# Kernel optimization log

Hardware: AMD Instinct MI355X
Metric: run time of the kernel (lower is better)

## Reference

```python
import jax, jax.numpy as jnp
import numpy as np

B, CIN, H, W = 128, 64, 32, 32
COUT, K, STRIDE, PAD = 64, 3, 1, 1
HO = (H + 2 * PAD - K) // STRIDE + 1
WO = (W + 2 * PAD - K) // STRIDE + 1


def setup_inputs() -> dict:
    key = jax.random.key(0)
    k1, k2 = jax.random.split(key)
    x = jax.random.normal(k1, (B, CIN, H, W), dtype=jnp.float32)
    # weight scaled like torch init: randn / sqrt(k*k*Cin) (orthogonal_ in torch just
    # re-orthogonalizes; scale here matches the fan-in normalization)
    weight = jax.random.normal(k2, (HO, WO, COUT, CIN, K, K), dtype=jnp.float32) / np.sqrt(K * K * CIN)
    bias = jnp.full((COUT, HO, WO), 0.5, dtype=jnp.float32)
    return {"x": x, "weight": weight, "bias": bias}


def reference(x, weight, bias):
    # pad spatial dims
    xp = jnp.pad(x, ((0, 0), (0, 0), (PAD, PAD), (PAD, PAD)))
    # gather row windows: [B, C, Ho, K, Wp]
    ri = (jnp.arange(HO) * STRIDE)[:, None] + jnp.arange(K)[None, :]  # [Ho, K]
    ci = (jnp.arange(WO) * STRIDE)[:, None] + jnp.arange(K)[None, :]  # [Wo, K]
    rows = xp[:, :, ri, :]           # [B, C, Ho, K, Wp]
    patches = rows[:, :, :, :, ci]   # [B, C, Ho, K, Wo, K]
    # per-location matmul: b c h p w q , h w d c p q -> b d h w
    out = jnp.einsum('bchpwq,hwdcpq->bdhw', patches, weight)
    return out + bias[None]
```

## Files before the change

kernel.cpp:

```cpp
#include <hip/hip_runtime.h>
#include <hip/hip_bf16.h>

#define KT 576

typedef __attribute__((ext_vector_type(8))) short  short8;
typedef __attribute__((ext_vector_type(4))) float  f32x4;

#define VMCNT(n) asm volatile("s_waitcnt vmcnt(" #n ")" ::: "memory")
#define SB() __builtin_amdgcn_sched_barrier(0)

__device__ __forceinline__ unsigned short f2bf(float f) {
  union { float f; unsigned int u; } v; v.f = f;
  return (unsigned short)((v.u + 0x7FFFu + ((v.u >> 16) & 1u)) >> 16);
}

__global__ __launch_bounds__(256) void xC2_kernel(const float* __restrict__ x,
                                                  unsigned short* __restrict__ xC2) {
  const int hp = blockIdx.x, bb = blockIdx.y, t = threadIdx.x;
  __shared__ unsigned short tile[32 * 1024];
  const bool interior = (hp >= 1 && hp <= 32);
  if (interior) {
#pragma unroll 4
    for (int i = 0; i < 32; ++i) {
      const int row = i * 32 + (t >> 3);
      const int bl = row >> 6, c = row & 63;
      const int k = t & 7;
      const float4 v = *(const float4*)(x + ((size_t)(bb * 16 + bl) * 64 + c) * 1024 +
                                        (hp - 1) * 32 + k * 4);
      const int base = (k * 4) * 1024 + (c >> 3) * 128 + bl * 8 + (c & 7);
      tile[base]        = f2bf(v.x);
      tile[base + 1024] = f2bf(v.y);
      tile[base + 2048] = f2bf(v.z);
      tile[base + 3072] = f2bf(v.w);
    }
  }
  __syncthreads();
  unsigned short* dst = xC2 + (size_t)hp * 278528 + (size_t)bb * 1024;
  const uint4 z = make_uint4(0u, 0u, 0u, 0u);
  for (int idx = t; idx < 34 * 128; idx += 256) {
    const int wp = idx >> 7, s = idx & 127;
    uint4 v = z;
    if (interior && wp >= 1 && wp <= 32) v = *(const uint4*)&tile[(wp - 1) * 1024 + s * 8];
    *(uint4*)(dst + (size_t)wp * 8192 + s * 8) = v;
  }
}

__global__ __launch_bounds__(256, 1) void lc_main(const float* __restrict__ Wt,
                                                  const float* __restrict__ bias,
                                                  const unsigned short* __restrict__ xC2,
                                                  float* __restrict__ out) {
  __shared__ unsigned short Wl[2][32 * KT];
  __shared__ float blds[128];

  const int bid = (int)blockIdx.x;
  const int swz = (bid & 7) * 64 + (bid >> 3);
  const int h = swz >> 4, rem = swz & 15, wq = rem >> 1, half = rem & 1;
  const int t = threadIdx.x, lane = t & 63, wv = t >> 6;
  const int l15 = lane & 15, lg = lane >> 4;

  if (t < 128)
    blds[t] = bias[(half * 32 + (t & 31)) * 1024 + h * 32 + wq * 4 + (t >> 5)];

  const unsigned short* xA = xC2 + (size_t)wv * 2048 + lg * 128 + l15 * 8;
  const int x7 = l15 & 7;
  const int wrow0 = l15 * KT;
  const int wrow1 = (16 + l15) * KT;

  f32x4 acc[4][2][2];
#pragma unroll
  for (int j = 0; j < 4; ++j)
#pragma unroll
    for (int bt = 0; bt < 2; ++bt)
#pragma unroll
      for (int dt = 0; dt < 2; ++dt) acc[j][bt][dt] = (f32x4){0.f, 0.f, 0.f, 0.f};

  short8 As0[3][3], As1[3][3];
  float4 wreg[18];

#define ISSUE_W(jj)                                                           \
  {                                                                           \
    const float* ws = Wt + (size_t)(h * 32 + wq * 4 + (jj)) * (64 * KT) +     \
                      (size_t)half * (32 * KT);                               \
    _Pragma("unroll")                                                         \
    for (int i = 0; i < 18; ++i) {                                            \
      const float4* p = (const float4*)ws + (i * 256 + t);                    \
      asm volatile("global_load_dwordx4 %0, %1, off" : "=v"(wreg[i]) : "v"(p)); \
    }                                                                         \
  }

#define ISSUE_A(K)                                                            \
  {                                                                           \
    _Pragma("unroll")                                                         \
    for (int s = 0; s < 3; ++s) {                                             \
      const int step = ((K) % 6) * 3 + s;                                     \
      const int pq = step >> 1, p = pq / 3, q = pq - p * 3;                   \
      const size_t off = (size_t)(h + p) * 278528 +                           \
                         (size_t)(wq * 4 + (K) / 6 + q) * 8192 + (step & 1) * 512; \
      const short8* p0 = (const short8*)(xA + off);                           \
      const short8* p1 = (const short8*)(xA + off + 1024);                    \
      asm volatile("global_load_dwordx4 %0, %1, off" : "=v"(As0[(K) % 3][s]) : "v"(p0)); \
      asm volatile("global_load_dwordx4 %0, %1, off" : "=v"(As1[(K) % 3][s]) : "v"(p1)); \
    }                                                                         \
  }

#define SCATTER(buf)                                                          \
  {                                                                           \
    _Pragma("unroll")                                                         \
    for (int i = 0; i < 18; ++i) {                                            \
      const int f = (i * 256 + t) * 4;                                        \
      const int d = (((unsigned)(f >> 6)) * 7282u) >> 16;                     \
      int kn = f - d * 576;                                                   \
      int c = ((unsigned)kn * 7282u) >> 16;                                   \
      int r = kn - c * 9;                                                     \
      const float vv[4] = {wreg[i].x, wreg[i].y, wreg[i].z, wreg[i].w};       \
      _Pragma("unroll")                                                       \
      for (int jx = 0; jx < 4; ++jx) {                                        \
        const int kp = r * 64 + c;                                            \
        const int slot = (kp >> 3) ^ (d & 7);                                 \
        Wl[buf][d * KT + slot * 8 + (kp & 7)] = f2bf(vv[jx]);                 \
        if (++r == 9) { r = 0; ++c; }                                         \
      }                                                                       \
    }                                                                         \
  }

#define STEP(jj, gg, NN)                                                      \
  {                                                                           \
    VMCNT(NN);                                                                \
    SB();                                                                     \
    _Pragma("unroll")                                                         \
    for (int s = 0; s < 3; ++s) {                                             \
      const int sb = ((gg) * 3 + s) * 4 + lg;                                 \
      const short8 b0 = *(const short8*)&Wl[(jj) & 1][wrow0 + ((sb ^ x7) << 3)]; \
      const short8 b1 = *(const short8*)&Wl[(jj) & 1][wrow1 + ((sb ^ x7) << 3)]; \
      acc[(jj)][0][0] = __builtin_amdgcn_mfma_f32_16x16x32_bf16(As0[((jj) * 6 + (gg)) % 3][s], b0, acc[(jj)][0][0], 0, 0, 0); \
      acc[(jj)][1][0] = __builtin_amdgcn_mfma_f32_16x16x32_bf16(As1[((jj) * 6 + (gg)) % 3][s], b0, acc[(jj)][1][0], 0, 0, 0); \
      acc[(jj)][0][1] = __builtin_amdgcn_mfma_f32_16x16x32_bf16(As0[((jj) * 6 + (gg)) % 3][s], b1, acc[(jj)][0][1], 0, 0, 0); \
      acc[(jj)][1][1] = __builtin_amdgcn_mfma_f32_16x16x32_bf16(As1[((jj) * 6 + (gg)) % 3][s], b1, acc[(jj)][1][1], 0, 0, 0); \
    }                                                                         \
  }

  ISSUE_W(0);
  ISSUE_A(0); ISSUE_A(1); ISSUE_A(2);
  VMCNT(18);
  SB();
  SCATTER(0);
  __syncthreads();

  ISSUE_W(1);
  STEP(0, 0, 30); ISSUE_A(3);
  STEP(0, 1, 30); ISSUE_A(4);
  STEP(0, 2, 30); ISSUE_A(5);
  STEP(0, 3, 12); ISSUE_A(6);
  STEP(0, 4, 12); ISSUE_A(7);
  STEP(0, 5, 12); ISSUE_A(8);
  SCATTER(1);
  __syncthreads();

  ISSUE_W(2);
  STEP(1, 0, 30); ISSUE_A(9);
  STEP(1, 1, 30); ISSUE_A(10);
  STEP(1, 2, 30); ISSUE_A(11);
  STEP(1, 3, 12); ISSUE_A(12);
  STEP(1, 4, 12); ISSUE_A(13);
  STEP(1, 5, 12); ISSUE_A(14);
  SCATTER(0);
  __syncthreads();

  ISSUE_W(3);
  STEP(2, 0, 30); ISSUE_A(15);
  STEP(2, 1, 30); ISSUE_A(16);
  STEP(2, 2, 30); ISSUE_A(17);
  STEP(2, 3, 12); ISSUE_A(18);
  STEP(2, 4, 12); ISSUE_A(19);
  STEP(2, 5, 12); ISSUE_A(20);
  SCATTER(1);
  __syncthreads();

  STEP(3, 0, 12); ISSUE_A(21);
  STEP(3, 1, 12); ISSUE_A(22);
  STEP(3, 2, 12); ISSUE_A(23);
  STEP(3, 3, 12);
  STEP(3, 4, 6);
  STEP(3, 5, 0);

#pragma unroll
  for (int dt = 0; dt < 2; ++dt) {
    const int dd = dt * 16 + l15;
    const int dg = half * 32 + dd;
    const float bv0 = blds[dd], bv1 = blds[32 + dd], bv2 = blds[64 + dd], bv3 = blds[96 + dd];
#pragma unroll
    for (int bt = 0; bt < 2; ++bt) {
#pragma unroll
      for (int i = 0; i < 4; ++i) {
        const int b = wv * 32 + bt * 16 + lg * 4 + i;
        float4 v;
        v.x = acc[0][bt][dt][i] + bv0;
        v.y = acc[1][bt][dt][i] + bv1;
        v.z = acc[2][bt][dt][i] + bv2;
        v.w = acc[3][bt][dt][i] + bv3;
        *(float4*)(out + (size_t)b * 65536 + (size_t)dg * 1024 + h * 32 + wq * 4) = v;
      }
    }
  }
}

extern "C" void kernel_launch(void* const* d_in, const int* in_sizes, int n_in,
                              void* d_out, int out_size, void* d_ws, size_t ws_size,
                              hipStream_t stream) {
  const float* x    = (const float*)d_in[0];
  const float* wt   = (const float*)d_in[1];
  const float* bias = (const float*)d_in[2];
  float* out        = (float*)d_out;
  unsigned short* xC2 = (unsigned short*)d_ws;

  xC2_kernel<<<dim3(34, 8), 256, 0, stream>>>(x, xC2);
  lc_main<<<512, 256, 0, stream>>>(wt, bias, xC2, out);
}
```

Baseline: 68.54 us.

## Split output channels into quarters per block to double grid and occupancy

Each block now covers 16 output channels instead of 32, so the grid doubles to 1024 blocks with half the LDS, half the weight registers, and launch bounds allowing two blocks per CU. The weight slice per block halves, and the wait counts are adjusted for the smaller weight issue. The cost is that the activation (A) fragments are now loaded twice as often across blocks, since each block reloads the same x tiles for fewer output channels.

```diff
diff --git a/kernel.cpp b/kernel.cpp
--- a/kernel.cpp
+++ b/kernel.cpp
@@ -45,44 +45,41 @@
   }
 }
 
-__global__ __launch_bounds__(256, 1) void lc_main(const float* __restrict__ Wt,
+__global__ __launch_bounds__(256, 2) void lc_main(const float* __restrict__ Wt,
                                                   const float* __restrict__ bias,
                                                   const unsigned short* __restrict__ xC2,
                                                   float* __restrict__ out) {
-  __shared__ unsigned short Wl[2][32 * KT];
-  __shared__ float blds[128];
+  __shared__ unsigned short Wl[2][16 * KT];
+  __shared__ float blds[64];
 
   const int bid = (int)blockIdx.x;
-  const int swz = (bid & 7) * 64 + (bid >> 3);
-  const int h = swz >> 4, rem = swz & 15, wq = rem >> 1, half = rem & 1;
+  const int swz = (bid & 7) * 128 + (bid >> 3);
+  const int quad = swz & 3, wq = (swz >> 2) & 7, h = swz >> 5;
   const int t = threadIdx.x, lane = t & 63, wv = t >> 6;
   const int l15 = lane & 15, lg = lane >> 4;
 
-  if (t < 128)
-    blds[t] = bias[(half * 32 + (t & 31)) * 1024 + h * 32 + wq * 4 + (t >> 5)];
+  if (t < 64)
+    blds[t] = bias[(quad * 16 + (t & 15)) * 1024 + h * 32 + wq * 4 + (t >> 4)];
 
   const unsigned short* xA = xC2 + (size_t)wv * 2048 + lg * 128 + l15 * 8;
   const int x7 = l15 & 7;
-  const int wrow0 = l15 * KT;
-  const int wrow1 = (16 + l15) * KT;
-
-  f32x4 acc[4][2][2];
+  const int wrow = l15 * KT;
+
+  f32x4 acc[4][2];
 #pragma unroll
   for (int j = 0; j < 4; ++j)
 #pragma unroll
-    for (int bt = 0; bt < 2; ++bt)
-#pragma unroll
-      for (int dt = 0; dt < 2; ++dt) acc[j][bt][dt] = (f32x4){0.f, 0.f, 0.f, 0.f};
+    for (int bt = 0; bt < 2; ++bt) acc[j][bt] = (f32x4){0.f, 0.f, 0.f, 0.f};
 
   short8 As0[3][3], As1[3][3];
-  float4 wreg[18];
+  float4 wreg[9];
 
 #define ISSUE_W(jj)                                                           \
   {                                                                           \
-    const float* ws = Wt + (size_t)(h * 32 + wq * 4 + (jj)) * (64 * KT) +     \
-                      (size_t)half * (32 * KT);                               \
-    _Pragma("unroll")                                                         \
-    for (int i = 0; i < 18; ++i) {                                            \
+    const float* ws = Wt + ((size_t)(h * 32 + wq * 4 + (jj)) * 64 +           \
+                            quad * 16) * KT;                                  \
+    _Pragma("unroll")                                                         \
+    for (int i = 0; i < 9; ++i) {                                             \
       const float4* p = (const float4*)ws + (i * 256 + t);                    \
       asm volatile("global_load_dwordx4 %0, %1, off" : "=v"(wreg[i]) : "v"(p)); \
     }                                                                         \
@@ -106,7 +103,7 @@
 #define SCATTER(buf)                                                          \
   {                                                                           \
     _Pragma("unroll")                                                         \
-    for (int i = 0; i < 18; ++i) {                                            \
+    for (int i = 0; i < 9; ++i) {                                             \
       const int f = (i * 256 + t) * 4;                                        \
       const int d = (((unsigned)(f >> 6)) * 7282u) >> 16;                     \
       int kn = f - d * 576;                                                   \
@@ -130,12 +127,9 @@
     _Pragma("unroll")                                                         \
     for (int s = 0; s < 3; ++s) {                                             \
       const int sb = ((gg) * 3 + s) * 4 + lg;                                 \
-      const short8 b0 = *(const short8*)&Wl[(jj) & 1][wrow0 + ((sb ^ x7) << 3)]; \
-      const short8 b1 = *(const short8*)&Wl[(jj) & 1][wrow1 + ((sb ^ x7) << 3)]; \
-      acc[(jj)][0][0] = __builtin_amdgcn_mfma_f32_16x16x32_bf16(As0[((jj) * 6 + (gg)) % 3][s], b0, acc[(jj)][0][0], 0, 0, 0); \
-      acc[(jj)][1][0] = __builtin_amdgcn_mfma_f32_16x16x32_bf16(As1[((jj) * 6 + (gg)) % 3][s], b0, acc[(jj)][1][0], 0, 0, 0); \
-      acc[(jj)][0][1] = __builtin_amdgcn_mfma_f32_16x16x32_bf16(As0[((jj) * 6 + (gg)) % 3][s], b1, acc[(jj)][0][1], 0, 0, 0); \
-      acc[(jj)][1][1] = __builtin_amdgcn_mfma_f32_16x16x32_bf16(As1[((jj) * 6 + (gg)) % 3][s], b1, acc[(jj)][1][1], 0, 0, 0); \
+      const short8 b0 = *(const short8*)&Wl[(jj) & 1][wrow + ((sb ^ x7) << 3)]; \
+      acc[(jj)][0] = __builtin_amdgcn_mfma_f32_16x16x32_bf16(As0[((jj) * 6 + (gg)) % 3][s], b0, acc[(jj)][0], 0, 0, 0); \
+      acc[(jj)][1] = __builtin_amdgcn_mfma_f32_16x16x32_bf16(As1[((jj) * 6 + (gg)) % 3][s], b0, acc[(jj)][1], 0, 0, 0); \
     }                                                                         \
   }
 
@@ -147,9 +141,9 @@
   __syncthreads();
 
   ISSUE_W(1);
-  STEP(0, 0, 30); ISSUE_A(3);
-  STEP(0, 1, 30); ISSUE_A(4);
-  STEP(0, 2, 30); ISSUE_A(5);
+  STEP(0, 0, 21); ISSUE_A(3);
+  STEP(0, 1, 21); ISSUE_A(4);
+  STEP(0, 2, 21); ISSUE_A(5);
   STEP(0, 3, 12); ISSUE_A(6);
   STEP(0, 4, 12); ISSUE_A(7);
   STEP(0, 5, 12); ISSUE_A(8);
@@ -157,9 +151,9 @@
   __syncthreads();
 
   ISSUE_W(2);
-  STEP(1, 0, 30); ISSUE_A(9);
-  STEP(1, 1, 30); ISSUE_A(10);
-  STEP(1, 2, 30); ISSUE_A(11);
+  STEP(1, 0, 21); ISSUE_A(9);
+  STEP(1, 1, 21); ISSUE_A(10);
+  STEP(1, 2, 21); ISSUE_A(11);
   STEP(1, 3, 12); ISSUE_A(12);
   STEP(1, 4, 12); ISSUE_A(13);
   STEP(1, 5, 12); ISSUE_A(14);
@@ -167,9 +161,9 @@
   __syncthreads();
 
   ISSUE_W(3);
-  STEP(2, 0, 30); ISSUE_A(15);
-  STEP(2, 1, 30); ISSUE_A(16);
-  STEP(2, 2, 30); ISSUE_A(17);
+  STEP(2, 0, 21); ISSUE_A(15);
+  STEP(2, 1, 21); ISSUE_A(16);
+  STEP(2, 2, 21); ISSUE_A(17);
   STEP(2, 3, 12); ISSUE_A(18);
   STEP(2, 4, 12); ISSUE_A(19);
   STEP(2, 5, 12); ISSUE_A(20);
@@ -184,22 +178,17 @@
   STEP(3, 5, 0);
 
 #pragma unroll
-  for (int dt = 0; dt < 2; ++dt) {
-    const int dd = dt * 16 + l15;
-    const int dg = half * 32 + dd;
-    const float bv0 = blds[dd], bv1 = blds[32 + dd], bv2 = blds[64 + dd], bv3 = blds[96 + dd];
-#pragma unroll
-    for (int bt = 0; bt < 2; ++bt) {
-#pragma unroll
-      for (int i = 0; i < 4; ++i) {
-        const int b = wv * 32 + bt * 16 + lg * 4 + i;
-        float4 v;
-        v.x = acc[0][bt][dt][i] + bv0;
-        v.y = acc[1][bt][dt][i] + bv1;
-        v.z = acc[2][bt][dt][i] + bv2;
-        v.w = acc[3][bt][dt][i] + bv3;
-        *(float4*)(out + (size_t)b * 65536 + (size_t)dg * 1024 + h * 32 + wq * 4) = v;
-      }
+  for (int bt = 0; bt < 2; ++bt) {
+#pragma unroll
+    for (int i = 0; i < 4; ++i) {
+      const int b = wv * 32 + bt * 16 + lg * 4 + i;
+      const int dg = quad * 16 + l15;
+      float4 v;
+      v.x = acc[0][bt][i] + blds[l15];
+      v.y = acc[1][bt][i] + blds[16 + l15];
+      v.z = acc[2][bt][i] + blds[32 + l15];
+      v.w = acc[3][bt][i] + blds[48 + l15];
+      *(float4*)(out + (size_t)b * 65536 + (size_t)dg * 1024 + h * 32 + wq * 4) = v;
     }
   }
 }
@@ -214,5 +203,5 @@
   unsigned short* xC2 = (unsigned short*)d_ws;
 
   xC2_kernel<<<dim3(34, 8), 256, 0, stream>>>(x, xC2);
-  lc_main<<<512, 256, 0, stream>>>(wt, bias, xC2, out);
-}
+  lc_main<<<1024, 256, 0, stream>>>(wt, bias, xC2, out);
+}
```

New measurement: 104.7 us. 52.7% more time.

## Halve weight staging registers for two blocks per CU, transpose output via temp

Applied to the files above, without the earlier changes.

Weight prefetch and scatter are split into two halves of 9 float4 registers instead of 18, and launch bounds are raised to allow two blocks per CU, aiming to overlap more memory latency. When the workspace is large enough, the epilogue writes accumulators contiguously to a temporary buffer and a new transpose kernel produces coalesced NCHW output. This replaces the old strided float4 stores but adds an extra kernel launch and a round trip of 32 MB through memory. LDS use is about 73 KB per block, which may limit whether two blocks actually fit.

```diff
diff --git a/kernel.cpp b/kernel.cpp
--- a/kernel.cpp
+++ b/kernel.cpp
@@ -45,10 +45,12 @@
   }
 }
 
-__global__ __launch_bounds__(256, 1) void lc_main(const float* __restrict__ Wt,
+__global__ __launch_bounds__(256, 2) void lc_main(const float* __restrict__ Wt,
                                                   const float* __restrict__ bias,
                                                   const unsigned short* __restrict__ xC2,
-                                                  float* __restrict__ out) {
+                                                  float* __restrict__ out,
+                                                  float* __restrict__ tmp,
+                                                  int useTmp) {
   __shared__ unsigned short Wl[2][32 * KT];
   __shared__ float blds[128];
 
@@ -75,15 +77,15 @@
       for (int dt = 0; dt < 2; ++dt) acc[j][bt][dt] = (f32x4){0.f, 0.f, 0.f, 0.f};
 
   short8 As0[3][3], As1[3][3];
-  float4 wreg[18];
-
-#define ISSUE_W(jj)                                                           \
+  float4 wreg[9];
+
+#define ISSUE_W9(jj, hs)                                                      \
   {                                                                           \
     const float* ws = Wt + (size_t)(h * 32 + wq * 4 + (jj)) * (64 * KT) +     \
                       (size_t)half * (32 * KT);                               \
     _Pragma("unroll")                                                         \
-    for (int i = 0; i < 18; ++i) {                                            \
-      const float4* p = (const float4*)ws + (i * 256 + t);                    \
+    for (int i = 0; i < 9; ++i) {                                             \
+      const float4* p = (const float4*)ws + (((hs) * 9 + i) * 256 + t);       \
       asm volatile("global_load_dwordx4 %0, %1, off" : "=v"(wreg[i]) : "v"(p)); \
     }                                                                         \
   }
@@ -103,11 +105,11 @@
     }                                                                         \
   }
 
-#define SCATTER(buf)                                                          \
-  {                                                                           \
-    _Pragma("unroll")                                                         \
-    for (int i = 0; i < 18; ++i) {                                            \
-      const int f = (i * 256 + t) * 4;                                        \
+#define SCATTER9(buf, hs)                                                     \
+  {                                                                           \
+    _Pragma("unroll")                                                         \
+    for (int i = 0; i < 9; ++i) {                                             \
+      const int f = ((((hs) * 9) + i) * 256 + t) * 4;                         \
       const int d = (((unsigned)(f >> 6)) * 7282u) >> 16;                     \
       int kn = f - d * 576;                                                   \
       int c = ((unsigned)kn * 7282u) >> 16;                                   \
@@ -139,42 +141,29 @@
     }                                                                         \
   }
 
-  ISSUE_W(0);
+#define PHASE(jj)                                                             \
+  ISSUE_W9(jj + 1, 0);                                                        \
+  STEP(jj, 0, 21); ISSUE_A(6 * (jj) + 3);                                     \
+  STEP(jj, 1, 21); ISSUE_A(6 * (jj) + 4);                                     \
+  STEP(jj, 2, 21); ISSUE_A(6 * (jj) + 5);                                     \
+  VMCNT(18); SB(); SCATTER9((jj + 1) & 1, 0);                                 \
+  ISSUE_W9(jj + 1, 1);                                                        \
+  STEP(jj, 3, 21); ISSUE_A(6 * (jj) + 6);                                     \
+  STEP(jj, 4, 21); ISSUE_A(6 * (jj) + 7);                                     \
+  STEP(jj, 5, 21); ISSUE_A(6 * (jj) + 8);                                     \
+  VMCNT(18); SB(); SCATTER9((jj + 1) & 1, 1);                                 \
+  __syncthreads();
+
+  ISSUE_W9(0, 0);
   ISSUE_A(0); ISSUE_A(1); ISSUE_A(2);
-  VMCNT(18);
-  SB();
-  SCATTER(0);
-  __syncthreads();
-
-  ISSUE_W(1);
-  STEP(0, 0, 30); ISSUE_A(3);
-  STEP(0, 1, 30); ISSUE_A(4);
-  STEP(0, 2, 30); ISSUE_A(5);
-  STEP(0, 3, 12); ISSUE_A(6);
-  STEP(0, 4, 12); ISSUE_A(7);
-  STEP(0, 5, 12); ISSUE_A(8);
-  SCATTER(1);
-  __syncthreads();
-
-  ISSUE_W(2);
-  STEP(1, 0, 30); ISSUE_A(9);
-  STEP(1, 1, 30); ISSUE_A(10);
-  STEP(1, 2, 30); ISSUE_A(11);
-  STEP(1, 3, 12); ISSUE_A(12);
-  STEP(1, 4, 12); ISSUE_A(13);
-  STEP(1, 5, 12); ISSUE_A(14);
-  SCATTER(0);
-  __syncthreads();
-
-  ISSUE_W(3);
-  STEP(2, 0, 30); ISSUE_A(15);
-  STEP(2, 1, 30); ISSUE_A(16);
-  STEP(2, 2, 30); ISSUE_A(17);
-  STEP(2, 3, 12); ISSUE_A(18);
-  STEP(2, 4, 12); ISSUE_A(19);
-  STEP(2, 5, 12); ISSUE_A(20);
-  SCATTER(1);
-  __syncthreads();
+  VMCNT(18); SB(); SCATTER9(0, 0);
+  ISSUE_W9(0, 1);
+  VMCNT(0);  SB(); SCATTER9(0, 1);
+  __syncthreads();
+
+  PHASE(0)
+  PHASE(1)
+  PHASE(2)
 
   STEP(3, 0, 12); ISSUE_A(21);
   STEP(3, 1, 12); ISSUE_A(22);
@@ -183,24 +172,68 @@
   STEP(3, 4, 6);
   STEP(3, 5, 0);
 
-#pragma unroll
-  for (int dt = 0; dt < 2; ++dt) {
-    const int dd = dt * 16 + l15;
-    const int dg = half * 32 + dd;
-    const float bv0 = blds[dd], bv1 = blds[32 + dd], bv2 = blds[64 + dd], bv3 = blds[96 + dd];
-#pragma unroll
-    for (int bt = 0; bt < 2; ++bt) {
-#pragma unroll
-      for (int i = 0; i < 4; ++i) {
-        const int b = wv * 32 + bt * 16 + lg * 4 + i;
-        float4 v;
-        v.x = acc[0][bt][dt][i] + bv0;
-        v.y = acc[1][bt][dt][i] + bv1;
-        v.z = acc[2][bt][dt][i] + bv2;
-        v.w = acc[3][bt][dt][i] + bv3;
-        *(float4*)(out + (size_t)b * 65536 + (size_t)dg * 1024 + h * 32 + wq * 4) = v;
+  if (useTmp) {
+#pragma unroll
+    for (int j = 0; j < 4; ++j) {
+      float* tb = tmp + (size_t)((h * 32 + wq * 4 + j) * 2 + half) * (32 * 128) + wv * 32;
+#pragma unroll
+      for (int dt = 0; dt < 2; ++dt) {
+        const float bv = blds[(j << 5) + dt * 16 + l15];
+#pragma unroll
+        for (int bt = 0; bt < 2; ++bt) {
+          f32x4 v = acc[j][bt][dt];
+          v[0] += bv; v[1] += bv; v[2] += bv; v[3] += bv;
+          *(f32x4*)(tb + (dt * 16 + l15) * 128 + bt * 16 + lg * 4) = v;
+        }
       }
     }
+  } else {
+#pragma unroll
+    for (int j = 0; j < 4; ++j) {
+      const int hw = h * 32 + wq * 4 + j;
+#pragma unroll
+      for (int dt = 0; dt < 2; ++dt) {
+        const int dg = half * 32 + dt * 16 + l15;
+        const float bv = blds[(j << 5) + dt * 16 + l15];
+#pragma unroll
+        for (int bt = 0; bt < 2; ++bt) {
+#pragma unroll
+          for (int i = 0; i < 4; ++i) {
+            const int b = wv * 32 + bt * 16 + lg * 4 + i;
+            out[(size_t)b * 65536 + (size_t)dg * 1024 + hw] = acc[j][bt][dt][i] + bv;
+          }
+        }
+      }
+    }
+  }
+}
+
+__global__ __launch_bounds__(256) void tr_out(const float* __restrict__ tmp,
+                                              float* __restrict__ out) {
+  const int h = blockIdx.x;
+  const int d = blockIdx.y;
+  const int half = d >> 5, dl = d & 31;
+  const int t = threadIdx.x;
+  __shared__ float ls[32 * 132];
+  {
+    const int w = t >> 3, bc = t & 7;
+    const float* src = tmp + ((size_t)((h * 32 + w) * 2 + half) * 32 + dl) * 128 + bc * 16;
+    float* dst = ls + w * 132 + bc * 16;
+#pragma unroll
+    for (int k = 0; k < 4; ++k) ((float4*)dst)[k] = ((const float4*)src)[k];
+  }
+  __syncthreads();
+  {
+    const int b = t >> 1, wh = t & 1;
+    float4 o[4];
+#pragma unroll
+    for (int k = 0; k < 4; ++k)
+#pragma unroll
+      for (int j = 0; j < 4; ++j)
+        ((float*)&o[k])[j] = ls[(wh * 16 + k * 4 + j) * 132 + b];
+    float* dst = out + (size_t)b * 65536 + (size_t)d * 1024 + h * 32 + wh * 16;
+#pragma unroll
+    for (int k = 0; k < 4; ++k) ((float4*)dst)[k] = o[k];
   }
 }
 
@@ -211,8 +244,14 @@
   const float* wt   = (const float*)d_in[1];
   const float* bias = (const float*)d_in[2];
   float* out        = (float*)d_out;
+
   unsigned short* xC2 = (unsigned short*)d_ws;
+  const size_t XC2_BYTES = 18939904u;
+  const size_t TMP_BYTES = 33554432u;
+  const int useTmp = (ws_size >= XC2_BYTES + TMP_BYTES) ? 1 : 0;
+  float* tmp = (float*)((char*)d_ws + XC2_BYTES);
 
   xC2_kernel<<<dim3(34, 8), 256, 0, stream>>>(x, xC2);
-  lc_main<<<512, 256, 0, stream>>>(wt, bias, xC2, out);
-}
+  lc_main<<<512, 256, 0, stream>>>(wt, bias, xC2, out, tmp, useTmp);
+  if (useTmp) tr_out<<<dim3(32, 64), 256, 0, stream>>>(tmp, out);
+}
```

New measurement: 115.2 us. 1.68x slower.

## Interleave weight prefetch in small chunks with MFMA steps instead of bursts

Applied to the files above, without the earlier changes.

The 18-load burst of weight prefetches per output column is split into six 3-load chunks, each issued alongside the activation loads between MFMA steps. The vmcnt waits are retuned to match, and some steps skip the wait because their data is already resident. The goal is to spread global memory traffic more evenly, so the weight burst no longer delays the first activation loads of each phase. It risks miscounted vmcnt values, which would give wrong results, and more in-flight register pressure.

```diff
diff --git a/kernel.cpp b/kernel.cpp
--- a/kernel.cpp
+++ b/kernel.cpp
@@ -77,7 +77,7 @@
   short8 As0[3][3], As1[3][3];
   float4 wreg[18];
 
-#define ISSUE_W(jj)                                                           \
+#define ISSUE_W18(jj)                                                         \
   {                                                                           \
     const float* ws = Wt + (size_t)(h * 32 + wq * 4 + (jj)) * (64 * KT) +     \
                       (size_t)half * (32 * KT);                               \
@@ -85,6 +85,17 @@
     for (int i = 0; i < 18; ++i) {                                            \
       const float4* p = (const float4*)ws + (i * 256 + t);                    \
       asm volatile("global_load_dwordx4 %0, %1, off" : "=v"(wreg[i]) : "v"(p)); \
+    }                                                                         \
+  }
+
+#define ISSUE_W3(jj, ck)                                                      \
+  {                                                                           \
+    const float* ws = Wt + (size_t)(h * 32 + wq * 4 + (jj)) * (64 * KT) +     \
+                      (size_t)half * (32 * KT);                               \
+    _Pragma("unroll")                                                         \
+    for (int i = 0; i < 3; ++i) {                                             \
+      const float4* p = (const float4*)ws + (((ck) * 3 + i) * 256 + t);       \
+      asm volatile("global_load_dwordx4 %0, %1, off" : "=v"(wreg[(ck) * 3 + i]) : "v"(p)); \
     }                                                                         \
   }
 
@@ -123,10 +134,8 @@
     }                                                                         \
   }
 
-#define STEP(jj, gg, NN)                                                      \
-  {                                                                           \
-    VMCNT(NN);                                                                \
-    SB();                                                                     \
+#define MFMAS(jj, gg)                                                         \
+  {                                                                           \
     _Pragma("unroll")                                                         \
     for (int s = 0; s < 3; ++s) {                                             \
       const int sb = ((gg) * 3 + s) * 4 + lg;                                 \
@@ -139,45 +148,44 @@
     }                                                                         \
   }
 
-  ISSUE_W(0);
+#define STEP(jj, gg, NN) { VMCNT(NN); SB(); MFMAS(jj, gg) }
+#define STEPNW(jj, gg)   { SB(); MFMAS(jj, gg) }
+
+  ISSUE_W18(0);
   ISSUE_A(0); ISSUE_A(1); ISSUE_A(2);
-  VMCNT(18);
-  SB();
+  VMCNT(18); SB();
   SCATTER(0);
-  __syncthreads();
-
-  ISSUE_W(1);
-  STEP(0, 0, 30); ISSUE_A(3);
-  STEP(0, 1, 30); ISSUE_A(4);
-  STEP(0, 2, 30); ISSUE_A(5);
-  STEP(0, 3, 12); ISSUE_A(6);
-  STEP(0, 4, 12); ISSUE_A(7);
-  STEP(0, 5, 12); ISSUE_A(8);
-  SCATTER(1);
-  __syncthreads();
-
-  ISSUE_W(2);
-  STEP(1, 0, 30); ISSUE_A(9);
-  STEP(1, 1, 30); ISSUE_A(10);
-  STEP(1, 2, 30); ISSUE_A(11);
-  STEP(1, 3, 12); ISSUE_A(12);
-  STEP(1, 4, 12); ISSUE_A(13);
-  STEP(1, 5, 12); ISSUE_A(14);
-  SCATTER(0);
-  __syncthreads();
-
-  ISSUE_W(3);
-  STEP(2, 0, 30); ISSUE_A(15);
-  STEP(2, 1, 30); ISSUE_A(16);
-  STEP(2, 2, 30); ISSUE_A(17);
-  STEP(2, 3, 12); ISSUE_A(18);
-  STEP(2, 4, 12); ISSUE_A(19);
-  STEP(2, 5, 12); ISSUE_A(20);
-  SCATTER(1);
-  __syncthreads();
-
-  STEP(3, 0, 12); ISSUE_A(21);
-  STEP(3, 1, 12); ISSUE_A(22);
+  __syncthreads(); SB();
+
+  STEP(0, 0, 12); ISSUE_A(3); ISSUE_W3(1, 0);
+  STEP(0, 1, 15); ISSUE_A(4); ISSUE_W3(1, 1);
+  STEP(0, 2, 18); ISSUE_A(5); ISSUE_W3(1, 2);
+  STEP(0, 3, 21); ISSUE_W3(1, 3); ISSUE_A(6);
+  STEP(0, 4, 21); ISSUE_W3(1, 4); ISSUE_A(7);
+  STEP(0, 5, 21); ISSUE_W3(1, 5); ISSUE_A(8);
+  VMCNT(6); SB(); SCATTER(1);
+  __syncthreads(); SB();
+
+  STEPNW(1, 0);   ISSUE_A(9);  ISSUE_W3(2, 0);
+  STEPNW(1, 1);   ISSUE_A(10); ISSUE_W3(2, 1);
+  STEP(1, 2, 18); ISSUE_A(11); ISSUE_W3(2, 2);
+  STEP(1, 3, 21); ISSUE_W3(2, 3); ISSUE_A(12);
+  STEP(1, 4, 21); ISSUE_W3(2, 4); ISSUE_A(13);
+  STEP(1, 5, 21); ISSUE_W3(2, 5); ISSUE_A(14);
+  VMCNT(6); SB(); SCATTER(0);
+  __syncthreads(); SB();
+
+  STEPNW(2, 0);   ISSUE_A(15); ISSUE_W3(3, 0);
+  STEPNW(2, 1);   ISSUE_A(16); ISSUE_W3(3, 1);
+  STEP(2, 2, 18); ISSUE_A(17); ISSUE_W3(3, 2);
+  STEP(2, 3, 21); ISSUE_W3(3, 3); ISSUE_A(18);
+  STEP(2, 4, 21); ISSUE_W3(3, 4); ISSUE_A(19);
+  STEP(2, 5, 21); ISSUE_W3(3, 5); ISSUE_A(20);
+  VMCNT(6); SB(); SCATTER(1);
+  __syncthreads(); SB();
+
+  STEPNW(3, 0);   ISSUE_A(21);
+  STEPNW(3, 1);   ISSUE_A(22);
   STEP(3, 2, 12); ISSUE_A(23);
   STEP(3, 3, 12);
   STEP(3, 4, 6);
```

After: 70.37 us. +2.7%, slower.
